# Performance work log

Measured on AMD Instinct MI355X. Metric: run time of the kernel, lower is better.

The kernel has to match this reference:

```python
import jax, jax.numpy as jnp
import numpy as np

S, T, B = 50, 50, 64
SRC_V, TRG_V = 36616, 23262
E, EH, DH = 300, 512, 1024


def setup_inputs() -> dict:
    key = jax.random.key(0)
    ks = jax.random.split(key, 20)
    n = lambda k, shape: jax.random.normal(k, shape, jnp.float32) * 0.05
    return {
        "train_src_batch": jax.random.randint(ks[0], (S, B), 0, SRC_V),
        "train_trg_batch": jax.random.randint(ks[1], (T, B), 0, TRG_V),
        "emb_en": n(ks[2], (SRC_V, E)),
        "emb_de": n(ks[3], (TRG_V, E)),
        "enc_W_ih_f": n(ks[4], (4 * EH, E)),
        "enc_W_hh_f": n(ks[5], (4 * EH, EH)),
        "enc_b_f": n(ks[6], (4 * EH,)),
        "enc_W_ih_b": n(ks[7], (4 * EH, E)),
        "enc_W_hh_b": n(ks[8], (4 * EH, EH)),
        "enc_b_b": n(ks[9], (4 * EH,)),
        "dec_W_ih": n(ks[10], (4 * DH, E + DH)),
        "dec_W_hh": n(ks[11], (4 * DH, DH)),
        "dec_b": n(ks[12], (4 * DH,)),
        "W_gen": n(ks[13], (TRG_V, DH)),
        "b_gen": n(ks[14], (TRG_V,)),
        "W_i": n(ks[15], (DH, DH)),
        "W_o": n(ks[16], (DH, 2 * DH)),
    }


def _lstm_step(x, h, c, W_ih, W_hh, b):
    # PyTorch gate order: i, f, g, o
    gates = x @ W_ih.T + h @ W_hh.T + b
    i, f, g, o = jnp.split(gates, 4, axis=-1)
    c_new = jax.nn.sigmoid(f) * c + jax.nn.sigmoid(i) * jnp.tanh(g)
    h_new = jax.nn.sigmoid(o) * jnp.tanh(c_new)
    return h_new, c_new


def _run_lstm(x_seq, W_ih, W_hh, b, hidden):
    h0 = jnp.zeros((x_seq.shape[1], hidden), x_seq.dtype)
    def step(carry, x):
        h, c = carry
        h, c = _lstm_step(x, h, c, W_ih, W_hh, b)
        return (h, c), h
    (h, c), hs = jax.lax.scan(step, (h0, h0), x_seq)
    return hs, h, c


def _forward(train_src_batch, train_trg_batch, emb_en, emb_de,
             enc_W_ih_f, enc_W_hh_f, enc_b_f, enc_W_ih_b, enc_W_hh_b, enc_b_b,
             dec_W_ih, dec_W_hh, dec_b, W_gen, b_gen, W_i, W_o):
    x = emb_en[train_src_batch]                       # [S,B,E]
    hs_f, hf, cf = _run_lstm(x, enc_W_ih_f, enc_W_hh_f, enc_b_f, EH)
    hs_b, hb, cb = _run_lstm(x[::-1], enc_W_ih_b, enc_W_hh_b, enc_b_b, EH)
    output_hs = jnp.concatenate([hs_f, hs_b[::-1]], axis=-1)  # [S,B,1024]
    # Faithful to h.contiguous().view(B,1024) on direction-major [2,B,512]
    h = jnp.reshape(jnp.stack([hf, hb], axis=0), (B, DH))
    c = jnp.reshape(jnp.stack([cf, cb], axis=0), (B, DH))

    emb_trg = emb_de[train_trg_batch[: T - 1]]        # [T-1,B,E]

    def step(carry, e):
        h, c = carry
        # score[j,b] = output_hs[j,b] . (W_i h[b])  (the diag of the original mm)
        scores = jnp.einsum('sbd,bd->sb', output_hs, h @ W_i.T)
        # legacy nn.Softmax() on 2D input -> softmax over dim=1 (batch axis)
        a = jax.nn.softmax(scores, axis=1)
        s_t = jnp.einsum('sb,sbd->bd', a, output_hs)
        c_t = jnp.tanh(jnp.concatenate([s_t, h], axis=1) @ W_o.T)
        dec_in = jnp.concatenate([c_t, e], axis=1)    # [B, 1024+300]
        h, c = _lstm_step(dec_in, h, c, dec_W_ih, dec_W_hh, dec_b)
        logp = jax.nn.log_softmax(h @ W_gen.T + b_gen, axis=1)
        return (h, c), logp

    _, outs = jax.lax.scan(step, (h, c), emb_trg)     # [T-1,B,V]
    out0 = jnp.zeros((1, B, TRG_V), outs.dtype)       # output[0] filled with 0
    return jnp.concatenate([out0, outs], axis=0)      # [T,B,V]


def reference(train_src_batch, train_trg_batch, emb_en, emb_de,
              enc_W_ih_f, enc_W_hh_f, enc_b_f, enc_W_ih_b, enc_W_hh_b, enc_b_b,
              dec_W_ih, dec_W_hh, dec_b, W_gen, b_gen, W_i, W_o):
    return _forward(train_src_batch, train_trg_batch, emb_en, emb_de,
                    enc_W_ih_f, enc_W_hh_f, enc_b_f, enc_W_ih_b, enc_W_hh_b, enc_b_b,
                    dec_W_ih, dec_W_hh, dec_b, W_gen, b_gen, W_i, W_o)
```

## Files before the change

### kernel.cpp

```cpp
#include <hip/hip_runtime.h>
#include <hip/hip_bf16.h>

#define SS 50
#define TT 50
#define BB 64
#define TRGV 23262
#define EE 300
#define EH 512
#define DH 1024

#define GMRE 3136
#define GMP 3200
#define GK 1024
#define GNRE TRGV
#define GNP 23296

typedef short bf16x8 __attribute__((ext_vector_type(8)));
typedef float f32x4 __attribute__((ext_vector_type(4)));

__device__ __forceinline__ void glds16(const void* g, void* l) {
  __builtin_amdgcn_global_load_lds(
      (const __attribute__((address_space(1))) void*)g,
      (__attribute__((address_space(3))) void*)l, 16, 0, 0);
}

__device__ __forceinline__ float sigm(float x) { return 1.f / (1.f + expf(-x)); }
__device__ __forceinline__ float sum4(f32x4 v) { return v[0] + v[1] + v[2] + v[3]; }

__device__ __forceinline__ void split2(float x, __hip_bfloat16& hi, __hip_bfloat16& lo) {
  hi = __float2bfloat16(x);
  lo = __float2bfloat16(x - __bfloat162float(hi));
}

__device__ __forceinline__ void gbarg(unsigned* arrive, unsigned* gen,
                                      int idxInGrp, int n, bool poller) {
  __syncthreads();
  unsigned g = __hip_atomic_load(gen, __ATOMIC_RELAXED, __HIP_MEMORY_SCOPE_AGENT);
  if (threadIdx.x == 0)
    __hip_atomic_store(arrive + idxInGrp * 16, g + 1u, __ATOMIC_RELEASE, __HIP_MEMORY_SCOPE_AGENT);
  if (poller) {
    int i = threadIdx.x;
    if (i < n) {
      while (__hip_atomic_load(arrive + i * 16, __ATOMIC_RELAXED, __HIP_MEMORY_SCOPE_AGENT) < g + 1u)
        __builtin_amdgcn_s_sleep(1);
      (void)__hip_atomic_load(arrive + i * 16, __ATOMIC_ACQUIRE, __HIP_MEMORY_SCOPE_AGENT);
    }
    __syncthreads();
    if (threadIdx.x == 0)
      __hip_atomic_store(gen, g + 1u, __ATOMIC_RELEASE, __HIP_MEMORY_SCOPE_AGENT);
  }
  if (threadIdx.x == 0) {
    while (__hip_atomic_load(gen, __ATOMIC_RELAXED, __HIP_MEMORY_SCOPE_AGENT) < g + 1u)
      __builtin_amdgcn_s_sleep(1);
    (void)__hip_atomic_load(gen, __ATOMIC_ACQUIRE, __HIP_MEMORY_SCOPE_AGENT);
  }
  __syncthreads();
}

__global__ void k_zero(float* __restrict__ p, long n) {
  long i = (long)blockIdx.x * 256 + threadIdx.x;
  if (i < n) p[i] = 0.f;
}
__global__ void k_zero_bf(__hip_bfloat16* __restrict__ p, long n) {
  long i = (long)blockIdx.x * 256 + threadIdx.x;
  if (i < n) p[i] = __float2bfloat16(0.f);
}

__global__ void k_embed(const int* __restrict__ src, const float* __restrict__ emb,
                        float* __restrict__ x) {
  int id = blockIdx.x * 256 + threadIdx.x;
  if (id >= SS * BB * EE) return;
  int sb = id / EE, e = id % EE;
  x[id] = emb[(long)src[sb] * EE + e];
}

__global__ void k_dbperm(const float* __restrict__ db, float* __restrict__ dbp) {
  int id = blockIdx.x * 256 + threadIdx.x;
  if (id >= 4096) return;
  int u = id >> 2, g = id & 3;
  dbp[id] = db[g * 1024 + u];
}

__global__ void k_split_pad(const float* __restrict__ in, int ld_in, int col_off,
                            int Kreal, int Kpad, int rows_real, long rows_pad,
                            int mode, __hip_bfloat16* __restrict__ out) {
  long id = (long)blockIdx.x * 256 + threadIdx.x;
  if (id >= rows_pad * Kpad) return;
  long r = id / Kpad;
  int k = id % Kpad;
  float v = 0.f;
  if (r < rows_real && k < Kreal) {
    if (mode == 3) {
      v = in[(long)k * ld_in + col_off + r];
    } else {
      long sr = r;
      if (mode == 1) sr = ((49 - (r >> 6)) << 6) + (r & 63);
      else if (mode == 2) sr = (long)(r & 3) * 1024 + (r >> 2);
      v = in[sr * ld_in + col_off + k];
    }
  }
  __hip_bfloat16 hi, lo;
  split2(v, hi, lo);
  out[r * 2 * Kpad + k] = hi;
  out[r * 2 * Kpad + Kpad + k] = lo;
}

__global__ void k_embgather_split(const int* __restrict__ trg, const float* __restrict__ emb,
                                  __hip_bfloat16* __restrict__ out) {
  long id = (long)blockIdx.x * 256 + threadIdx.x;
  if (id >= 3200L * 320) return;
  long r = id / 320;
  int k = id % 320;
  int t = r >> 6, b = r & 63;
  float v = 0.f;
  if (t < TT - 1 && k < EE) v = emb[(long)trg[t * BB + b] * EE + k];
  __hip_bfloat16 hi, lo;
  split2(v, hi, lo);
  out[r * 640 + k] = hi;
  out[r * 640 + 320 + k] = lo;
}

__global__ void k_tobf16_pad(const float* __restrict__ W, __hip_bfloat16* __restrict__ Wb,
                             long nrow_real, long nrow_pad, int K) {
  long id = (long)blockIdx.x * 256 + threadIdx.x;
  if (id >= nrow_pad * K) return;
  long r = id / K;
  Wb[id] = __float2bfloat16(r < nrow_real ? W[id] : 0.f);
}

__global__ void k_repackT(const float* __restrict__ in, float* __restrict__ out) {
  long id = (long)blockIdx.x * 256 + threadIdx.x;
  if (id >= 3200L * 1024) return;
  long r = id >> 10;
  int n = id & 1023;
  out[((long)(n >> 2) * 3200 + r) * 4 + (n & 3)] = in[id];
}

template<int OUTBF>
__global__ __launch_bounds__(256) void k_gsplit(
    const __hip_bfloat16* __restrict__ A2, const __hip_bfloat16* __restrict__ W2,
    const float* __restrict__ bias, void* __restrict__ Cout,
    int Mreal, int Nreal, int ldc, int Kpad) {
  __shared__ __hip_bfloat16 As[128 * 32];
  __shared__ __hip_bfloat16 Bs[128 * 32];
  int tid = threadIdx.x, lane = tid & 63, w = tid >> 6;
  long m0 = (long)blockIdx.y * 128, n0 = (long)blockIdx.x * 128;
  int lda2 = 2 * Kpad;
  int srow = lane >> 2;
  int scol = (lane & 3) * 8;
  char* lA0 = (char*)As + w * 2048;
  char* lA1 = lA0 + 1024;
  char* lB0 = (char*)Bs + w * 2048;
  char* lB1 = lB0 + 1024;
  int wm = (w >> 1) * 64, wn = (w & 1) * 64;
  int fr = lane & 15;
  int kc = (lane >> 4) * 8;
  f32x4 acc[4][4] = {};

  for (int seg = 0; seg < 3; ++seg) {
    const __hip_bfloat16* Ab = A2 + (seg == 1 ? Kpad : 0);
    const __hip_bfloat16* Wb = W2 + (seg == 2 ? Kpad : 0);
    const __hip_bfloat16* gA0 = Ab + (m0 + w * 32 + srow) * (long)lda2 + scol;
    const __hip_bfloat16* gA1 = gA0 + 16L * lda2;
    const __hip_bfloat16* gB0 = Wb + (n0 + w * 32 + srow) * (long)lda2 + scol;
    const __hip_bfloat16* gB1 = gB0 + 16L * lda2;
    for (int kt = 0; kt < Kpad / 32; ++kt) {
      int k0 = kt * 32;
      glds16(gA0 + k0, lA0);
      glds16(gA1 + k0, lA1);
      glds16(gB0 + k0, lB0);
      glds16(gB1 + k0, lB1);
      __syncthreads();
      bf16x8 a[4], b[4];
      for (int mi = 0; mi < 4; ++mi)
        a[mi] = *(const bf16x8*)(As + (wm + mi * 16 + fr) * 32 + kc);
      for (int ni = 0; ni < 4; ++ni)
        b[ni] = *(const bf16x8*)(Bs + (wn + ni * 16 + fr) * 32 + kc);
      for (int mi = 0; mi < 4; ++mi)
        for (int ni = 0; ni < 4; ++ni)
          acc[mi][ni] = __builtin_amdgcn_mfma_f32_16x16x32_bf16(a[mi], b[ni], acc[mi][ni], 0, 0, 0);
      __syncthreads();
    }
  }

  for (int mi = 0; mi < 4; ++mi) {
    for (int ni = 0; ni < 4; ++ni) {
      int n = (int)n0 + wn + ni * 16 + (lane & 15);
      if (n >= Nreal) continue;
      float bv = bias ? bias[n] : 0.f;
      for (int r = 0; r < 4; ++r) {
        int m = (int)m0 + wm + mi * 16 + (lane >> 4) * 4 + r;
        if (m >= Mreal) continue;
        float v = acc[mi][ni][r] + bv;
        if (OUTBF) ((__hip_bfloat16*)Cout)[(long)m * ldc + n] = __float2bfloat16(v);
        else ((float*)Cout)[(long)m * ldc + n] = v;
      }
    }
  }
}

__global__ __launch_bounds__(512) void persist_enc(
    const float* __restrict__ xW_f, const float* __restrict__ xW_b,
    const float* __restrict__ Whf, const float* __restrict__ Whb,
    float* __restrict__ hs, float* hA, float* hB, float* hA2, float* hB2,
    float* __restrict__ cf, float* __restrict__ cb,
    float* __restrict__ hd0, float* __restrict__ hT0, float* __restrict__ cdD,
    __hip_bfloat16* __restrict__ x2A, unsigned* __restrict__ bar) {
  __shared__ float WL[16 * 516];
  int t = threadIdx.x;
  int blk = blockIdx.x;
  int dir = blk >> 7, bl = blk & 127;
  const float* Whh = dir ? Whb : Whf;
  const float* xWb0 = dir ? xW_b : xW_f;
  float* c = dir ? cb : cf;
  float* hp = dir ? hA2 : hA;
  float* hn = dir ? hB2 : hB;
  unsigned* arrG = bar + dir * 2048;
  unsigned* genG = bar + 12288 + dir * 16;
  unsigned* arrA = bar + 4096;
  unsigned* genA = bar + 12320;

  for (int idx = t; idx < 16 * 512; idx += 512) {
    int r = idx >> 9, k = idx & 511;
    int srcrow = (r & 3) * 512 + (bl * 4 + (r >> 2));
    WL[r * 516 + k] = Whh[(long)srcrow * 512 + k];
  }
  __syncthreads();

  int j = t & 15;
  int b0 = t >> 4, b1 = b0 + 32;
  int g = j & 3;
  int ju = bl * 4 + (j >> 2);
  int lbase = (t & 63) & ~3;
  const f32x4* wq = (const f32x4*)(WL + j * 516);

  for (int s = 0; s < SS; ++s) {
    const f32x4* h0q = (const f32x4*)(hp + b0 * 512);
    const f32x4* h1q = (const f32x4*)(hp + b1 * 512);
    f32x4 v0 = {0, 0, 0, 0}, v1 = {0, 0, 0, 0};
    for (int q = 0; q < 128; ++q) {
      f32x4 wv = wq[q];
      v0 += wv * h0q[q];
      v1 += wv * h1q[q];
    }
    const float* xW = xWb0 + (long)(s * BB) * 2048;
    float a0 = sum4(v0) + xW[b0 * 2048 + g * 512 + ju];
    float a1 = sum4(v1) + xW[b1 * 2048 + g * 512 + ju];
    float gi0 = __shfl(a0, lbase + 0), gf0 = __shfl(a0, lbase + 1);
    float gg0 = __shfl(a0, lbase + 2), go0 = __shfl(a0, lbase + 3);
    float gi1 = __shfl(a1, lbase + 0), gf1 = __shfl(a1, lbase + 1);
    float gg1 = __shfl(a1, lbase + 2), go1 = __shfl(a1, lbase + 3);
    if ((t & 3) == 0) {
      int hscol = dir ? (512 + ju) : ju;
      int srow = dir ? (SS - 1 - s) : s;
      long hsrow0 = (long)(srow * BB + b0) * DH + hscol;
      long hsrow1 = (long)(srow * BB + b1) * DH + hscol;
      float cn0 = sigm(gf0) * c[b0 * 512 + ju] + sigm(gi0) * tanhf(gg0);
      float hn0 = sigm(go0) * tanhf(cn0);
      c[b0 * 512 + ju] = cn0;
      hn[b0 * 512 + ju] = hn0;
      hs[hsrow0] = hn0;
      float cn1 = sigm(gf1) * c[b1 * 512 + ju] + sigm(gi1) * tanhf(gg1);
      float hn1 = sigm(go1) * tanhf(cn1);
      c[b1 * 512 + ju] = cn1;
      hn[b1 * 512 + ju] = hn1;
      hs[hsrow1] = hn1;
    }
    float* tmp = hp; hp = hn; hn = tmp;
    gbarg(arrG, genG, bl, 128, bl == 0);
  }
  gbarg(arrA, genA, blk, 256, blk == 0);
  int gid = blk * 512 + t;
  if (gid < 65536) {
    int d2 = gid >> 15, b = (gid >> 9) & 63, j2 = gid & 511;
    float hv = (d2 ? hA2 : hA)[b * 512 + j2];
    float cv = (d2 ? cb : cf)[b * 512 + j2];
    hd0[gid] = hv;
    cdD[gid] = cv;
    int bp = gid >> 10, jp = gid & 1023;
    hT0[jp * 64 + bp] = hv;
    __hip_bfloat16 hi, lo;
    split2(hv, hi, lo);
    x2A[bp * 4096 + 1024 + jp] = hi;
    x2A[bp * 4096 + 3072 + jp] = lo;
  }
}

__global__ __launch_bounds__(1024) void persist_dec(
    const float* __restrict__ G, const float* __restrict__ HsWo1T,
    const float* __restrict__ Wo, const float* __restrict__ dWih,
    const float* __restrict__ dWhh, const __hip_bfloat16* __restrict__ Eg,
    float* hd0, float* hd1, float* hT0, float* hT1,
    float* __restrict__ cd, float* __restrict__ scoresG,
    __hip_bfloat16* __restrict__ A_bf,
    __hip_bfloat16* __restrict__ xA, __hip_bfloat16* __restrict__ xB,
    unsigned* __restrict__ bar) {
  __shared__ __hip_bfloat16 WB[512 * 128];
  __shared__ float Abuf[4096];
  int t = threadIdx.x;
  int blk = blockIdx.x;
  int w = t >> 6, lane = t & 63;
  unsigned* arrive = bar + 8192;
  unsigned* gen = bar + 12336;
  bool pol = (blk == 255);

  for (int idx = t; idx < 16 * 2048; idx += 1024) {
    int jj = idx >> 11;
    int k = idx & 2047;
    int rp2 = blk * 16 + jj;
    long srcrow = (long)(rp2 & 3) * 1024 + (rp2 >> 2);
    float v = (k < 1024) ? dWih[srcrow * 1324 + k] : dWhh[srcrow * 1024 + (k - 1024)];
    __hip_bfloat16 hi, lo;
    split2(v, hi, lo);
    WB[((k >> 3) * 16 + jj) * 8 + (k & 7)] = hi;
    WB[(((k + 2048) >> 3) * 16 + jj) * 8 + (k & 7)] = lo;
  }
  __syncthreads();

  float* hcur = hd0; float* hnew = hd1;
  float* hTc = hT0;  float* hTn = hT1;
  int j = t & 15, b = t >> 4;
  int rp = blk * 16 + j;
  int ju = blk * 4 + (j >> 2);
  int lbase = lane & ~3;
  const f32x4* hw4 = (const f32x4*)(HsWo1T + (long)blk * 3200 * 4);
  f32x4* Abuf4 = (f32x4*)Abuf;
  const float* wo2 = Wo + (long)(blk * 4) * 2048 + 1024;
  int mt = w & 3, kg = w >> 2;
  int row_a = mt * 16 + (lane & 15);
  int kq = lane >> 4;

  for (int ts = 0; ts < TT - 1; ++ts) {
    const __hip_bfloat16* xc = (ts & 1) ? xB : xA;
    __hip_bfloat16* xn = (ts & 1) ? xA : xB;
    float eg = __bfloat162float(Eg[((long)(ts * BB + b)) * 4096 + rp]);

    if (blk < 200) {
      int s = blk >> 2;
      int bb = (blk & 3) * 16 + (t >> 6);
      int ln = t & 63;
      const f32x4* gq = (const f32x4*)(G + ((long)s * 64 + bb) * 1024);
      const f32x4* hq = (const f32x4*)(hcur + bb * 1024);
      f32x4 a4 = {0, 0, 0, 0};
      #pragma unroll
      for (int q = 0; q < 4; ++q) a4 += gq[ln + q * 64] * hq[ln + q * 64];
      float p = sum4(a4);
      for (int o = 1; o < 64; o <<= 1) p += __shfl_xor(p, o);
      if (ln == 0) scoresG[s * 64 + bb] = p;
    }
    {
      f32x4 z1 = {0, 0, 0, 0};
      for (int k = w * 64; k < w * 64 + 64; ++k) {
        float hb = hTc[k * 64 + lane];
        f32x4 wv = {wo2[k], wo2[2048 + k], wo2[4096 + k], wo2[6144 + k]};
        z1 += hb * wv;
      }
      Abuf4[w * 64 + lane] = z1;
    }
    gbarg(arrive, gen, blk, 256, pol);

    {
      f32x4 z2 = {0, 0, 0, 0};
      for (int s = w; s < SS; s += 16) {
        float sc = scoresG[s * 64 + lane];
        float m = sc;
        for (int o = 32; o > 0; o >>= 1) m = fmaxf(m, __shfl_xor(m, o));
        float e = expf(sc - m);
        float su = e;
        for (int o = 32; o > 0; o >>= 1) su += __shfl_xor(su, o);
        z2 += (e / su) * hw4[s * 64 + lane];
      }
      Abuf4[w * 64 + lane] += z2;
      __syncthreads();
      if (t < 256) {
        int bb = t >> 2, nl = t & 3;
        float sv = 0.f;
        for (int i = 0; i < 16; ++i) sv += Abuf[(i * 64 + bb) * 4 + nl];
        float ct = tanhf(sv);
        __hip_bfloat16 hi, lo;
        split2(ct, hi, lo);
        ((__hip_bfloat16*)xc)[bb * 4096 + blk * 4 + nl] = hi;
        ((__hip_bfloat16*)xc)[bb * 4096 + 2048 + blk * 4 + nl] = lo;
      }
    }
    gbarg(arrive, gen, blk, 256, pol);

    {
      f32x4 acc = {0, 0, 0, 0};
      const __hip_bfloat16* xrow = xc + (long)row_a * 4096 + kq * 8;
      for (int seg = 0; seg < 3; ++seg) {
        int aoff = (seg == 1) ? 2048 : 0;
        int woff = (seg == 2) ? 2048 : 0;
        #pragma unroll
        for (int c = 0; c < 16; ++c) {
          int kb = kg * 512 + c * 32;
          bf16x8 a = *(const bf16x8*)(xrow + aoff + kb);
          int gidx = ((woff + kb) >> 3) + kq;
          bf16x8 bfr = *(const bf16x8*)(WB + (gidx * 16 + (lane & 15)) * 8);
          acc = __builtin_amdgcn_mfma_f32_16x16x32_bf16(a, bfr, acc, 0, 0, 0);
        }
      }
      for (int r = 0; r < 4; ++r)
        Abuf[kg * 1024 + (mt * 16 + kq * 4 + r) * 16 + (lane & 15)] = acc[r];
      __syncthreads();
      float gv = Abuf[t] + Abuf[1024 + t] + Abuf[2048 + t] + Abuf[3072 + t] + eg;
      float gi0 = __shfl(gv, lbase + 0), gf0 = __shfl(gv, lbase + 1);
      float gg0 = __shfl(gv, lbase + 2), go0 = __shfl(gv, lbase + 3);
      if ((t & 3) == 0) {
        float cn0 = sigm(gf0) * cd[b * DH + ju] + sigm(gi0) * tanhf(gg0);
        float hn0 = sigm(go0) * tanhf(cn0);
        cd[b * DH + ju] = cn0;
        hnew[b * DH + ju] = hn0;
        hTn[ju * 64 + b] = hn0;
        __hip_bfloat16 hi, lo;
        split2(hn0, hi, lo);
        A_bf[(long)ts * (BB * DH) + b * DH + ju] = hi;
        xn[b * 4096 + 1024 + ju] = hi;
        xn[b * 4096 + 3072 + ju] = lo;
      }
    }
    { float* x = hcur; hcur = hnew; hnew = x; }
    { float* x = hTc; hTc = hTn; hTn = x; }
    gbarg(arrive, gen, blk, 256, pol);
  }
}

__global__ __launch_bounds__(256) void k_gen_mfma(
    const __hip_bfloat16* __restrict__ A, const __hip_bfloat16* __restrict__ Bw,
    const float* __restrict__ bias, float* __restrict__ C) {
  __shared__ __hip_bfloat16 As[128 * 32];
  __shared__ __hip_bfloat16 Bs[128 * 32];
  int tid = threadIdx.x;
  int lane = tid & 63, w = tid >> 6;
  long m0 = (long)blockIdx.y * 128, n0 = (long)blockIdx.x * 128;
  int srow = lane >> 2;
  int scol = (lane & 3) * 8;
  const __hip_bfloat16* gA0 = A + (m0 + w * 32 + srow) * GK + scol;
  const __hip_bfloat16* gA1 = gA0 + 16 * GK;
  const __hip_bfloat16* gB0 = Bw + (n0 + w * 32 + srow) * GK + scol;
  const __hip_bfloat16* gB1 = gB0 + 16 * GK;
  char* lA0 = (char*)As + w * 2048;
  char* lA1 = lA0 + 1024;
  char* lB0 = (char*)Bs + w * 2048;
  char* lB1 = lB0 + 1024;
  int wm = (w >> 1) * 64, wn = (w & 1) * 64;
  int fr = lane & 15;
  int kc = (lane >> 4) * 8;
  f32x4 acc[4][4] = {};
  for (int kt = 0; kt < GK / 32; ++kt) {
    int k0 = kt * 32;
    glds16(gA0 + k0, lA0);
    glds16(gA1 + k0, lA1);
    glds16(gB0 + k0, lB0);
    glds16(gB1 + k0, lB1);
    __syncthreads();
    bf16x8 a[4], b[4];
    for (int mi = 0; mi < 4; ++mi)
      a[mi] = *(const bf16x8*)(As + (wm + mi * 16 + fr) * 32 + kc);
    for (int ni = 0; ni < 4; ++ni)
      b[ni] = *(const bf16x8*)(Bs + (wn + ni * 16 + fr) * 32 + kc);
    for (int mi = 0; mi < 4; ++mi)
      for (int ni = 0; ni < 4; ++ni)
        acc[mi][ni] = __builtin_amdgcn_mfma_f32_16x16x32_bf16(a[mi], b[ni], acc[mi][ni], 0, 0, 0);
    __syncthreads();
  }
  for (int mi = 0; mi < 4; ++mi) {
    for (int ni = 0; ni < 4; ++ni) {
      int n = (int)n0 + wn + ni * 16 + (lane & 15);
      if (n >= GNRE) continue;
      float bv = bias[n];
      for (int r = 0; r < 4; ++r) {
        int m = (int)m0 + wm + mi * 16 + (lane >> 4) * 4 + r;
        if (m < GMRE) C[(long)m * TRGV + n] = acc[mi][ni][r] + bv;
      }
    }
  }
}

__global__ __launch_bounds__(256) void k_logsoftmax(float* __restrict__ out) {
  int r = blockIdx.x;
  float* p = out + (long)(BB + r) * TRGV;
  int tid = threadIdx.x;
  __shared__ float red[256];
  float m = -1e30f;
  for (int i = tid; i < TRGV; i += 256) m = fmaxf(m, p[i]);
  red[tid] = m;
  __syncthreads();
  for (int s = 128; s > 0; s >>= 1) {
    if (tid < s) red[tid] = fmaxf(red[tid], red[tid + s]);
    __syncthreads();
  }
  m = red[0];
  __syncthreads();
  float sum = 0.f;
  for (int i = tid; i < TRGV; i += 256) sum += expf(p[i] - m);
  red[tid] = sum;
  __syncthreads();
  for (int s = 128; s > 0; s >>= 1) {
    if (tid < s) red[tid] += red[tid + s];
    __syncthreads();
  }
  float lse = m + logf(red[0]);
  for (int i = tid; i < TRGV; i += 256) p[i] -= lse;
}

extern "C" void kernel_launch(void* const* d_in, const int* in_sizes, int n_in,
                              void* d_out, int out_size, void* d_ws, size_t ws_size,
                              hipStream_t stream) {
  const int* src = (const int*)d_in[0];
  const int* trg = (const int*)d_in[1];
  const float* emb_en = (const float*)d_in[2];
  const float* emb_de = (const float*)d_in[3];
  const float* eWih_f = (const float*)d_in[4];
  const float* eWhh_f = (const float*)d_in[5];
  const float* eb_f = (const float*)d_in[6];
  const float* eWih_b = (const float*)d_in[7];
  const float* eWhh_b = (const float*)d_in[8];
  const float* eb_b = (const float*)d_in[9];
  const float* dWih = (const float*)d_in[10];
  const float* dWhh = (const float*)d_in[11];
  const float* db = (const float*)d_in[12];
  const float* Wgen = (const float*)d_in[13];
  const float* bgen = (const float*)d_in[14];
  const float* Wi = (const float*)d_in[15];
  const float* Wo = (const float*)d_in[16];
  float* out = (float*)d_out;

  float* base = (float*)d_ws;
  __hip_bfloat16* xsf = (__hip_bfloat16*)base;
  __hip_bfloat16* xsb = (__hip_bfloat16*)(base + 1024000);
  __hip_bfloat16* Wihf2 = (__hip_bfloat16*)(base + 2048000);
  __hip_bfloat16* Wihb2 = (__hip_bfloat16*)(base + 2703360);
  float* xW_f = base + 3358720;
  float* xW_b = base + 9912320;
  __hip_bfloat16* hs2 = (__hip_bfloat16*)base;
  __hip_bfloat16* Wi2 = (__hip_bfloat16*)(base + 3276800);
  __hip_bfloat16* Wo12 = (__hip_bfloat16*)(base + 4325376);
  __hip_bfloat16* eg2 = (__hip_bfloat16*)(base + 5373952);
  __hip_bfloat16* Wce2 = (__hip_bfloat16*)(base + 6397952);
  __hip_bfloat16* E_g = (__hip_bfloat16*)(base + 7708672);
  __hip_bfloat16* Wgen_bf = (__hip_bfloat16*)base;
  float* p = base + 16465920;
  float* x_enc = p; p += SS * BB * EE;
  float* hs = p; p += (long)SS * BB * DH;
  float* G = p; p += (long)SS * BB * DH;
  float* HsWo1 = p; p += (long)SS * BB * DH;
  float* HsWo1T = p; p += (long)SS * BB * DH;
  __hip_bfloat16* A_bf = (__hip_bfloat16*)p; p += (GMP * GK) / 2;
  __hip_bfloat16* x2A = (__hip_bfloat16*)p; p += (BB * 4096) / 2;
  __hip_bfloat16* x2B = (__hip_bfloat16*)p; p += (BB * 4096) / 2;
  float* dbp = p; p += 4096;
  float* scoresG = p; p += SS * BB;
  float* hd0 = p; p += BB * DH;
  float* hd1 = p; p += BB * DH;
  float* hT0 = p; p += BB * DH;
  float* hT1 = p; p += BB * DH;
  float* cd = p; p += BB * DH;
  float* hA = p; p += BB * EH;
  float* hB = p; p += BB * EH;
  float* hA2 = p; p += BB * EH;
  float* hB2 = p; p += BB * EH;
  float* cf = p; p += BB * EH;
  float* cb = p; p += BB * EH;
  unsigned* bar = (unsigned*)p; p += 12352;

  dim3 b256(256);

  k_embed<<<dim3((SS * BB * EE + 255) / 256), b256, 0, stream>>>(src, emb_en, x_enc);
  k_zero<<<dim3((6 * BB * EH + 255) / 256), b256, 0, stream>>>(hA, 6 * BB * EH);
  k_zero<<<dim3(49), b256, 0, stream>>>((float*)bar, 12352);
  k_zero<<<dim3((int)(((long)BB * TRGV + 255) / 256)), b256, 0, stream>>>(out, (long)BB * TRGV);
  k_zero_bf<<<dim3(((GMP - GMRE) * GK + 255) / 256), b256, 0, stream>>>(
      A_bf + (long)GMRE * GK, (long)(GMP - GMRE) * GK);
  k_dbperm<<<dim3(16), b256, 0, stream>>>(db, dbp);

  k_split_pad<<<dim3((3200 * 320 + 255) / 256), b256, 0, stream>>>(
      x_enc, EE, 0, EE, 320, 3200, 3200, 0, xsf);
  k_split_pad<<<dim3((3200 * 320 + 255) / 256), b256, 0, stream>>>(
      x_enc, EE, 0, EE, 320, 3200, 3200, 1, xsb);
  k_split_pad<<<dim3((2048 * 320 + 255) / 256), b256, 0, stream>>>(
      eWih_f, EE, 0, EE, 320, 2048, 2048, 0, Wihf2);
  k_split_pad<<<dim3((2048 * 320 + 255) / 256), b256, 0, stream>>>(
      eWih_b, EE, 0, EE, 320, 2048, 2048, 0, Wihb2);
  k_gsplit<0><<<dim3(16, 25), b256, 0, stream>>>(xsf, Wihf2, eb_f, xW_f, 3200, 2048, 2048, 320);
  k_gsplit<0><<<dim3(16, 25), b256, 0, stream>>>(xsb, Wihb2, eb_b, xW_b, 3200, 2048, 2048, 320);

  {
    void* args[] = {(void*)&xW_f, (void*)&xW_b, (void*)&eWhh_f, (void*)&eWhh_b,
                    (void*)&hs, (void*)&hA, (void*)&hB, (void*)&hA2, (void*)&hB2,
                    (void*)&cf, (void*)&cb, (void*)&hd0, (void*)&hT0, (void*)&cd,
                    (void*)&x2A, (void*)&bar};
    hipLaunchCooperativeKernel((const void*)persist_enc, dim3(256), dim3(512),
                               args, 0, stream);
  }

  k_split_pad<<<dim3((int)((3200L * 1024 + 255) / 256)), b256, 0, stream>>>(
      hs, DH, 0, DH, 1024, 3200, 3200, 0, hs2);
  k_split_pad<<<dim3((int)((1024L * 1024 + 255) / 256)), b256, 0, stream>>>(
      Wi, DH, 0, DH, 1024, 1024, 1024, 3, Wi2);
  k_split_pad<<<dim3((int)((1024L * 1024 + 255) / 256)), b256, 0, stream>>>(
      Wo, 2 * DH, 0, DH, 1024, 1024, 1024, 0, Wo12);
  k_embgather_split<<<dim3((int)((3200L * 320 + 255) / 256)), b256, 0, stream>>>(
      trg, emb_de, eg2);
  k_split_pad<<<dim3((int)((4096L * 320 + 255) / 256)), b256, 0, stream>>>(
      dWih, 1324, 1024, EE, 320, 4096, 4096, 2, Wce2);
  k_gsplit<0><<<dim3(8, 25), b256, 0, stream>>>(hs2, Wi2, (const float*)nullptr, G, 3200, 1024, 1024, 1024);
  k_gsplit<0><<<dim3(8, 25), b256, 0, stream>>>(hs2, Wo12, (const float*)nullptr, HsWo1, 3200, 1024, 1024, 1024);
  k_repackT<<<dim3((int)((3200L * 1024 + 255) / 256)), b256, 0, stream>>>(HsWo1, HsWo1T);
  k_gsplit<1><<<dim3(32, 25), b256, 0, stream>>>(eg2, Wce2, dbp, E_g, 3136, 4096, 4096, 320);

  {
    void* args[] = {(void*)&G, (void*)&HsWo1T, (void*)&Wo, (void*)&dWih, (void*)&dWhh,
                    (void*)&E_g, (void*)&hd0, (void*)&hd1, (void*)&hT0, (void*)&hT1,
                    (void*)&cd, (void*)&scoresG, (void*)&A_bf, (void*)&x2A, (void*)&x2B,
                    (void*)&bar};
    hipLaunchCooperativeKernel((const void*)persist_dec, dim3(256), dim3(1024),
                               args, 0, stream);
  }

  k_tobf16_pad<<<dim3((int)(((long)GNP * GK + 255) / 256)), b256, 0, stream>>>(
      Wgen, Wgen_bf, GNRE, GNP, GK);
  k_gen_mfma<<<dim3(GNP / 128, GMP / 128), b256, 0, stream>>>(
      A_bf, Wgen_bf, bgen, out + (long)BB * TRGV);
  k_logsoftmax<<<dim3((TT - 1) * BB), b256, 0, stream>>>(out);
}
```

Baseline: 6.431 ms.

## Split decoder gate GEMM across K chunks with global partials and bf16 attention values

The persistent decoder's gate GEMM is reorganised. Each block now holds a 64-row by 512-K slice of the split-bf16 weights instead of 16 rows by the full K, and writes partial sums to a global gparts buffer. A fourth grid barrier per step then reduces those partials. The HsWo1T attention-value table is stored in bf16 to halve its read traffic, and the double-buffered h/x arrays become single in-place buffers. This trades an extra grid-wide barrier and global partial traffic for fewer redundant x reads per block. The bf16 values also add precision loss, and writing h in place while other blocks still read it in the same step risks a race.

```diff
diff --git a/kernel.cpp b/kernel.cpp
--- a/kernel.cpp
+++ b/kernel.cpp
@@ -26,6 +26,10 @@
 
 __device__ __forceinline__ float sigm(float x) { return 1.f / (1.f + expf(-x)); }
 __device__ __forceinline__ float sum4(f32x4 v) { return v[0] + v[1] + v[2] + v[3]; }
+__device__ __forceinline__ float bfu2f(unsigned short u) {
+  unsigned int x = ((unsigned)u) << 16;
+  return __uint_as_float(x);
+}
 
 __device__ __forceinline__ void split2(float x, __hip_bfloat16& hi, __hip_bfloat16& lo) {
   hi = __float2bfloat16(x);
@@ -128,12 +132,12 @@
   Wb[id] = __float2bfloat16(r < nrow_real ? W[id] : 0.f);
 }
 
-__global__ void k_repackT(const float* __restrict__ in, float* __restrict__ out) {
+__global__ void k_repackT(const float* __restrict__ in, __hip_bfloat16* __restrict__ out) {
   long id = (long)blockIdx.x * 256 + threadIdx.x;
   if (id >= 3200L * 1024) return;
   long r = id >> 10;
   int n = id & 1023;
-  out[((long)(n >> 2) * 3200 + r) * 4 + (n & 3)] = in[id];
+  out[((long)(n >> 2) * 3200 + r) * 4 + (n & 3)] = __float2bfloat16(in[id]);
 }
 
 template<int OUTBF>
@@ -287,15 +291,14 @@
 }
 
 __global__ __launch_bounds__(1024) void persist_dec(
-    const float* __restrict__ G, const float* __restrict__ HsWo1T,
+    const float* __restrict__ G, const __hip_bfloat16* __restrict__ HsWo1T,
     const float* __restrict__ Wo, const float* __restrict__ dWih,
     const float* __restrict__ dWhh, const __hip_bfloat16* __restrict__ Eg,
-    float* hd0, float* hd1, float* hT0, float* hT1,
+    float* __restrict__ h, float* __restrict__ hT,
     float* __restrict__ cd, float* __restrict__ scoresG,
-    __hip_bfloat16* __restrict__ A_bf,
-    __hip_bfloat16* __restrict__ xA, __hip_bfloat16* __restrict__ xB,
-    unsigned* __restrict__ bar) {
-  __shared__ __hip_bfloat16 WB[512 * 128];
+    __hip_bfloat16* __restrict__ A_bf, __hip_bfloat16* __restrict__ x,
+    float* __restrict__ gparts, unsigned* __restrict__ bar) {
+  __shared__ __hip_bfloat16 WB[65536];
   __shared__ float Abuf[4096];
   int t = threadIdx.x;
   int blk = blockIdx.x;
@@ -304,35 +307,38 @@
   unsigned* gen = bar + 12336;
   bool pol = (blk == 255);
 
-  for (int idx = t; idx < 16 * 2048; idx += 1024) {
-    int jj = idx >> 11;
-    int k = idx & 2047;
-    int rp2 = blk * 16 + jj;
+  int nblk = blk >> 2, kchunk = blk & 3;
+
+  for (int idx = t; idx < 64 * 512; idx += 1024) {
+    int r = idx >> 9;
+    int kk = idx & 511;
+    int rp2 = nblk * 64 + r;
     long srcrow = (long)(rp2 & 3) * 1024 + (rp2 >> 2);
-    float v = (k < 1024) ? dWih[srcrow * 1324 + k] : dWhh[srcrow * 1024 + (k - 1024)];
+    int kabs = kchunk * 512 + kk;
+    float v = (kabs < 1024) ? dWih[srcrow * 1324 + kabs]
+                            : dWhh[srcrow * 1024 + (kabs - 1024)];
     __hip_bfloat16 hi, lo;
     split2(v, hi, lo);
-    WB[((k >> 3) * 16 + jj) * 8 + (k & 7)] = hi;
-    WB[(((k + 2048) >> 3) * 16 + jj) * 8 + (k & 7)] = lo;
+    int c = kk >> 5, kq = (kk >> 3) & 3, e = kk & 7;
+    int nt = r >> 4, rr = r & 15;
+    WB[((((0 * 16 + c) * 4 + kq) * 4 + nt) * 16 + rr) * 8 + e] = hi;
+    WB[((((1 * 16 + c) * 4 + kq) * 4 + nt) * 16 + rr) * 8 + e] = lo;
   }
   __syncthreads();
 
-  float* hcur = hd0; float* hnew = hd1;
-  float* hTc = hT0;  float* hTn = hT1;
   int j = t & 15, b = t >> 4;
   int rp = blk * 16 + j;
-  int ju = blk * 4 + (j >> 2);
+  int nn = (blk & 3) * 16 + j;
+  int ju = rp >> 2;
   int lbase = lane & ~3;
-  const f32x4* hw4 = (const f32x4*)(HsWo1T + (long)blk * 3200 * 4);
+  const unsigned short* hwb = (const unsigned short*)HsWo1T + (long)blk * 3200 * 4;
   f32x4* Abuf4 = (f32x4*)Abuf;
   const float* wo2 = Wo + (long)(blk * 4) * 2048 + 1024;
-  int mt = w & 3, kg = w >> 2;
+  int mt = w & 3, nt = w >> 2;
   int row_a = mt * 16 + (lane & 15);
   int kq = lane >> 4;
 
   for (int ts = 0; ts < TT - 1; ++ts) {
-    const __hip_bfloat16* xc = (ts & 1) ? xB : xA;
-    __hip_bfloat16* xn = (ts & 1) ? xA : xB;
     float eg = __bfloat162float(Eg[((long)(ts * BB + b)) * 4096 + rp]);
 
     if (blk < 200) {
@@ -340,7 +346,7 @@
       int bb = (blk & 3) * 16 + (t >> 6);
       int ln = t & 63;
       const f32x4* gq = (const f32x4*)(G + ((long)s * 64 + bb) * 1024);
-      const f32x4* hq = (const f32x4*)(hcur + bb * 1024);
+      const f32x4* hq = (const f32x4*)(h + bb * 1024);
       f32x4 a4 = {0, 0, 0, 0};
       #pragma unroll
       for (int q = 0; q < 4; ++q) a4 += gq[ln + q * 64] * hq[ln + q * 64];
@@ -351,7 +357,7 @@
     {
       f32x4 z1 = {0, 0, 0, 0};
       for (int k = w * 64; k < w * 64 + 64; ++k) {
-        float hb = hTc[k * 64 + lane];
+        float hb = hT[k * 64 + lane];
         f32x4 wv = {wo2[k], wo2[2048 + k], wo2[4096 + k], wo2[6144 + k]};
         z1 += hb * wv;
       }
@@ -368,7 +374,9 @@
         float e = expf(sc - m);
         float su = e;
         for (int o = 32; o > 0; o >>= 1) su += __shfl_xor(su, o);
-        z2 += (e / su) * hw4[s * 64 + lane];
+        const unsigned short* u4 = hwb + ((long)s * 64 + lane) * 4;
+        f32x4 hv = {bfu2f(u4[0]), bfu2f(u4[1]), bfu2f(u4[2]), bfu2f(u4[3])};
+        z2 += (e / su) * hv;
       }
       Abuf4[w * 64 + lane] += z2;
       __syncthreads();
@@ -379,48 +387,56 @@
         float ct = tanhf(sv);
         __hip_bfloat16 hi, lo;
         split2(ct, hi, lo);
-        ((__hip_bfloat16*)xc)[bb * 4096 + blk * 4 + nl] = hi;
-        ((__hip_bfloat16*)xc)[bb * 4096 + 2048 + blk * 4 + nl] = lo;
+        x[bb * 4096 + blk * 4 + nl] = hi;
+        x[bb * 4096 + 2048 + blk * 4 + nl] = lo;
       }
     }
     gbarg(arrive, gen, blk, 256, pol);
 
     {
       f32x4 acc = {0, 0, 0, 0};
-      const __hip_bfloat16* xrow = xc + (long)row_a * 4096 + kq * 8;
-      for (int seg = 0; seg < 3; ++seg) {
-        int aoff = (seg == 1) ? 2048 : 0;
-        int woff = (seg == 2) ? 2048 : 0;
+      const __hip_bfloat16* xrow = x + (long)row_a * 4096 + kchunk * 512 + kq * 8;
+      #pragma unroll
+      for (int pass = 0; pass < 3; ++pass) {
+        int hh = (pass == 2) ? 1 : 0;
+        int wh = (pass == 1) ? 1 : 0;
+        const __hip_bfloat16* xp = xrow + hh * 2048;
+        const __hip_bfloat16* wp = WB + (((wh * 16) * 4 + kq) * 4 + nt) * 16 * 8;
         #pragma unroll
         for (int c = 0; c < 16; ++c) {
-          int kb = kg * 512 + c * 32;
-          bf16x8 a = *(const bf16x8*)(xrow + aoff + kb);
-          int gidx = ((woff + kb) >> 3) + kq;
-          bf16x8 bfr = *(const bf16x8*)(WB + (gidx * 16 + (lane & 15)) * 8);
+          bf16x8 a = *(const bf16x8*)(xp + c * 32);
+          bf16x8 bfr = *(const bf16x8*)(wp + (long)c * 4 * 4 * 16 * 8 + (lane & 15) * 8);
           acc = __builtin_amdgcn_mfma_f32_16x16x32_bf16(a, bfr, acc, 0, 0, 0);
         }
       }
-      for (int r = 0; r < 4; ++r)
-        Abuf[kg * 1024 + (mt * 16 + kq * 4 + r) * 16 + (lane & 15)] = acc[r];
-      __syncthreads();
-      float gv = Abuf[t] + Abuf[1024 + t] + Abuf[2048 + t] + Abuf[3072 + t] + eg;
+      float* gp = gparts + (long)blk * 4096;
+      for (int r = 0; r < 4; ++r) {
+        int m = mt * 16 + kq * 4 + r;
+        int n = nt * 16 + (lane & 15);
+        gp[m * 64 + n] = acc[r];
+      }
+    }
+    gbarg(arrive, gen, blk, 256, pol);
+
+    {
+      long gbase = (long)((blk >> 2) * 4) * 4096 + b * 64 + nn;
+      float gv = gparts[gbase] + gparts[gbase + 4096] +
+                 gparts[gbase + 2 * 4096] + gparts[gbase + 3 * 4096] + eg;
       float gi0 = __shfl(gv, lbase + 0), gf0 = __shfl(gv, lbase + 1);
       float gg0 = __shfl(gv, lbase + 2), go0 = __shfl(gv, lbase + 3);
       if ((t & 3) == 0) {
         float cn0 = sigm(gf0) * cd[b * DH + ju] + sigm(gi0) * tanhf(gg0);
         float hn0 = sigm(go0) * tanhf(cn0);
         cd[b * DH + ju] = cn0;
-        hnew[b * DH + ju] = hn0;
-        hTn[ju * 64 + b] = hn0;
+        h[b * DH + ju] = hn0;
+        hT[ju * 64 + b] = hn0;
         __hip_bfloat16 hi, lo;
         split2(hn0, hi, lo);
         A_bf[(long)ts * (BB * DH) + b * DH + ju] = hi;
-        xn[b * 4096 + 1024 + ju] = hi;
-        xn[b * 4096 + 3072 + ju] = lo;
-      }
-    }
-    { float* x = hcur; hcur = hnew; hnew = x; }
-    { float* x = hTc; hTc = hTn; hTn = x; }
+        x[b * 4096 + 1024 + ju] = hi;
+        x[b * 4096 + 3072 + ju] = lo;
+      }
+    }
     gbarg(arrive, gen, blk, 256, pol);
   }
 }
@@ -545,16 +561,14 @@
   float* hs = p; p += (long)SS * BB * DH;
   float* G = p; p += (long)SS * BB * DH;
   float* HsWo1 = p; p += (long)SS * BB * DH;
-  float* HsWo1T = p; p += (long)SS * BB * DH;
+  __hip_bfloat16* HsWo1T = (__hip_bfloat16*)p; p += (long)SS * BB * DH / 2;
   __hip_bfloat16* A_bf = (__hip_bfloat16*)p; p += (GMP * GK) / 2;
   __hip_bfloat16* x2A = (__hip_bfloat16*)p; p += (BB * 4096) / 2;
-  __hip_bfloat16* x2B = (__hip_bfloat16*)p; p += (BB * 4096) / 2;
+  float* gparts = p; p += 256 * 4096;
   float* dbp = p; p += 4096;
   float* scoresG = p; p += SS * BB;
   float* hd0 = p; p += BB * DH;
-  float* hd1 = p; p += BB * DH;
   float* hT0 = p; p += BB * DH;
-  float* hT1 = p; p += BB * DH;
   float* cd = p; p += BB * DH;
   float* hA = p; p += BB * EH;
   float* hB = p; p += BB * EH;
@@ -611,9 +625,8 @@
 
   {
     void* args[] = {(void*)&G, (void*)&HsWo1T, (void*)&Wo, (void*)&dWih, (void*)&dWhh,
-                    (void*)&E_g, (void*)&hd0, (void*)&hd1, (void*)&hT0, (void*)&hT1,
-                    (void*)&cd, (void*)&scoresG, (void*)&A_bf, (void*)&x2A, (void*)&x2B,
-                    (void*)&bar};
+                    (void*)&E_g, (void*)&hd0, (void*)&hT0, (void*)&cd, (void*)&scoresG,
+                    (void*)&A_bf, (void*)&x2A, (void*)&gparts, (void*)&bar};
     hipLaunchCooperativeKernel((const void*)persist_dec, dim3(256), dim3(1024),
                                args, 0, stream);
   }
```

After: 6.562 ms. 2.0% more time.
